# Kernel optimization log

Hardware: AMD Instinct MI355X
Metric: run time of the kernel (lower is better)

The kernel has to match this reference:

```python
import jax, jax.numpy as jnp
import numpy as np

WS = 8          # window size
DISP = 4        # ws // 2 cyclic shift displacement
WS2 = WS * WS   # tokens per window
HEADS = 3
HD = 32         # head dim
SCALE = HD ** -0.5


def _mask(upper_lower, left_right):
    m = np.zeros((WS2, WS2), np.float32)
    if upper_lower:
        m[-DISP * WS:, :-DISP * WS] = -np.inf
        m[:-DISP * WS, -DISP * WS:] = -np.inf
    if left_right:
        m = m.reshape(WS, WS, WS, WS)
        m[:, -DISP:, :, :-DISP] = -np.inf
        m[:, :-DISP, :, -DISP:] = -np.inf
        m = m.reshape(WS2, WS2)
    return m

UL = _mask(True, False)
LR = _mask(False, True)
_ix = np.array([(i, j) for i in range(WS) for j in range(WS)])
REL = (_ix[None] - _ix[:, None]) + WS - 1  # [WS2, WS2, 2] relative index table


def _ln(x, g, b):
    m = x.mean(-1, keepdims=True)
    v = ((x - m) ** 2).mean(-1, keepdims=True)
    return (x - m) * jax.lax.rsqrt(v + 1e-5) * g + b


def _wattn(x, Wqkv, pos, Wo, bo, shifted):
    if shifted:
        x = jnp.roll(x, (-DISP, -DISP), axis=(1, 2))
    b, H, W, _ = x.shape
    nh, nw = H // WS, W // WS
    # qkv: last dim laid out as (3, heads, head_dim) matching torch chunk + rearrange
    qkv = (x @ Wqkv).reshape(b, nh, WS, nw, WS, 3, HEADS, HD)
    qkv = qkv.transpose(5, 0, 6, 1, 3, 2, 4, 7).reshape(3, b, HEADS, nh * nw, WS2, HD)
    q, k, v = qkv[0], qkv[1], qkv[2]
    dots = jnp.einsum('bhwid,bhwjd->bhwij', q, k) * SCALE  # [b,h,nwin,ws2,ws2]
    dots = dots + pos[REL[..., 0], REL[..., 1]]            # relative pos bias
    if shifted:
        m = np.zeros((nh * nw, WS2, WS2), np.float32)
        m[-nw:] += UL             # windows in last row
        m[nw - 1::nw] += LR       # windows in last column
        dots = dots + jnp.asarray(m)[None, None]
    a = jax.nn.softmax(dots, axis=-1)
    o = jnp.einsum('bhwij,bhwjd->bhwid', a, v)
    o = o.reshape(b, HEADS, nh, nw, WS, WS, HD).transpose(0, 2, 4, 3, 5, 1, 6).reshape(b, H, W, HEADS * HD)
    o = o @ Wo + bo
    if shifted:
        o = jnp.roll(o, (DISP, DISP), axis=(1, 2))
    return o


def _block(t, g1, b1, Wqkv, pos, Wo, bo, g2, b2, W1, bf1, W2, bf2, shifted):
    t = t + _wattn(_ln(t, g1, b1), Wqkv, pos, Wo, bo, shifted)
    h = _ln(t, g2, b2)
    return t + (jax.nn.gelu(h @ W1 + bf1, approximate=False) @ W2 + bf2)


def _stage(x, Wm, bm, pa, pb):
    b, c, H, W = x.shape
    nh, nw = H // 2, W // 2
    # PatchMerging: Unfold(k=2,s=2) layout is (c, ki, kj) with c outermost
    t = x.reshape(b, c, nh, 2, nw, 2).transpose(0, 2, 4, 1, 3, 5).reshape(b, nh, nw, c * 4)
    t = t @ Wm + bm
    t = _block(t, *pa, False)
    t = _block(t, *pb, True)
    return t.transpose(0, 3, 1, 2)


def setup_inputs() -> dict:
    key = jax.random.key(0)
    ks = jax.random.split(key, 12)
    def w(k, shp):
        return jax.random.normal(k, shp, jnp.float32) * 0.02
    def blk(kw, kp, ko, k1, k2):
        return {'g1': jnp.ones((128,), jnp.float32), 'b1': jnp.zeros((128,), jnp.float32),
                'Wqkv': w(kw, (128, 288)), 'pos': jax.random.normal(kp, (15, 15), jnp.float32),
                'Wo': w(ko, (96, 128)), 'bo': jnp.zeros((128,), jnp.float32),
                'g2': jnp.ones((128,), jnp.float32), 'b2': jnp.zeros((128,), jnp.float32),
                'W1': w(k1, (128, 512)), 'bf1': jnp.zeros((512,), jnp.float32),
                'W2': w(k2, (512, 128)), 'bf2': jnp.zeros((128,), jnp.float32)}
    A = blk(ks[2], ks[3], ks[4], ks[5], ks[6])
    B = blk(ks[7], ks[8], ks[9], ks[10], ks[11])
    inp = {'x': jax.random.normal(ks[0], (8, 64, 256, 256), jnp.float32),
           'Wm': w(ks[1], (256, 128)), 'bm': jnp.zeros((128,), jnp.float32)}
    for n, v in A.items():
        inp[n + 'a'] = v
    for n, v in B.items():
        inp[n + 'b'] = v
    return inp


def reference(x, Wm, bm, g1a, b1a, Wqkva, posa, Woa, boa, g2a, b2a, W1a, bf1a, W2a, bf2a,
              g1b, b1b, Wqkvb, posb, Wob, bob, g2b, b2b, W1b, bf1b, W2b, bf2b):
    pa = (g1a, b1a, Wqkva, posa, Woa, boa, g2a, b2a, W1a, bf1a, W2a, bf2a)
    pb = (g1b, b1b, Wqkvb, posb, Wob, bob, g2b, b2b, W1b, bf1b, W2b, bf2b)
    return _stage(x, Wm, bm, pa, pb)
```

## Files before the change

kernel.cpp:

```cpp
#include <hip/hip_runtime.h>
#include <math.h>

#define Timg 131072
#define SCALE 0.17677669529663689f

typedef __attribute__((ext_vector_type(8))) short frag8;
typedef __attribute__((ext_vector_type(8))) unsigned short us8;
typedef __attribute__((ext_vector_type(4))) float f32x4;

__device__ inline float bf2f(unsigned short u) {
    union { unsigned int i; float f; } v; v.i = ((unsigned int)u) << 16; return v.f;
}
__device__ inline unsigned short f2bf(float f) {
    union { float f; unsigned int i; } v; v.f = f;
    unsigned int r = v.i + 0x7fff + ((v.i >> 16) & 1);
    return (unsigned short)(r >> 16);
}
__device__ inline unsigned int pk2(float lo, float hi) {
    return ((unsigned int)f2bf(hi) << 16) | (unsigned int)f2bf(lo);
}
__device__ inline float gelu_f(float x) {
    float u = x * x;
    float z = x * fmaf(u, 0.044715f, 1.0f);
    float e = __builtin_amdgcn_exp2f(-2.3025851f * z);
    return x * __builtin_amdgcn_rcpf(1.f + e);
}

__global__ __launch_bounds__(256) void k_wcvt(
    const float* __restrict__ src, unsigned short* __restrict__ dst, int R, int C,
    int qrows, float s)
{
    int idx = blockIdx.x * 256 + threadIdx.x;
    if (idx >= R * C) return;
    int r = idx / C, c = idx % C;
    float v = src[idx];
    if (c < qrows) v *= s;
    dst[(size_t)c * R + r] = f2bf(v);
}

#define LDA_PM 264
__global__ __launch_bounds__(256) void k_patchmerge(
    const float* __restrict__ x, const unsigned short* __restrict__ Wmt,
    const float* __restrict__ bm, float* __restrict__ t)
{
    __shared__ unsigned short A[64 * LDA_PM];
    int blk = blockIdx.x;
    int b   = blk >> 8;
    int rem = blk & 255;
    int h   = rem >> 1;
    int w0  = (rem & 1) * 64;
    int tid = threadIdx.x;
    {
        int row = tid >> 1, half = tid & 1;
        int c = row >> 1, ki = row & 1;
        const float* src = x + (((size_t)(b*64 + c))*256 + (size_t)(2*h + ki))*256 + 2*w0 + half*64;
        int base = c*4 + ki*2;
        #pragma unroll
        for (int q = 0; q < 16; ++q) {
            float4 v = *reinterpret_cast<const float4*>(src + q*4);
            int tk0 = (half*64 + q*4) >> 1;
            *reinterpret_cast<unsigned int*>(&A[ tk0     * LDA_PM + base]) = pk2(v.x, v.y);
            *reinterpret_cast<unsigned int*>(&A[(tk0 + 1)* LDA_PM + base]) = pk2(v.z, v.w);
        }
    }
    __syncthreads();
    int lane = tid & 63, w = tid >> 6;
    int lr = lane & 15, lg = lane >> 4;
    size_t tok0 = (size_t)blk * 64;
    #pragma unroll
    for (int nt = 0; nt < 2; ++nt) {
        int n0 = (w*2 + nt) * 16;
        f32x4 acc[4] = {};
        #pragma unroll
        for (int ks = 0; ks < 8; ++ks) {
            frag8 bfr = *reinterpret_cast<const frag8*>(Wmt + (size_t)(n0 + lr)*256 + ks*32 + lg*8);
            #pragma unroll
            for (int m = 0; m < 4; ++m) {
                frag8 af = *reinterpret_cast<const frag8*>(&A[(m*16 + lr)*LDA_PM + ks*32 + lg*8]);
                acc[m] = __builtin_amdgcn_mfma_f32_16x16x32_bf16(af, bfr, acc[m], 0, 0, 0);
            }
        }
        #pragma unroll
        for (int m = 0; m < 4; ++m)
            #pragma unroll
            for (int r = 0; r < 4; ++r) {
                int rowl = m*16 + lg*4 + r;
                int col  = n0 + lr;
                t[(tok0 + rowl)*128 + col] = acc[m][r] + bm[col];
            }
    }
}

#define LDQK 200
#define LDVT 72
#define LDP  72
#define LDAO 104
#define LDA  136
#define LDH  136
#define OFF_VT  25600
#define OFF_HC1 17408
#define R1SZ    39424
#define OFF_AO  48640
#define SMEMSZ  61952
__global__ __launch_bounds__(256) void k_block(
    const float* __restrict__ pos, float* __restrict__ t,
    const float* __restrict__ g1, const float* __restrict__ b1,
    const unsigned short* __restrict__ Wqt,
    const unsigned short* __restrict__ Wot, const float* __restrict__ bo,
    const float* __restrict__ g2, const float* __restrict__ b2,
    const unsigned short* __restrict__ W1t, const float* __restrict__ bf1,
    const unsigned short* __restrict__ W2t, const float* __restrict__ bf2,
    int shifted)
{
    __shared__ __attribute__((aligned(16))) char smem[SMEMSZ];
    __shared__ float stats[64][4][2];
    __shared__ float ps[225];
    unsigned short* QK   = (unsigned short*)(smem);
    unsigned short* Vt   = (unsigned short*)(smem + OFF_VT);
    unsigned short* Hc0  = (unsigned short*)(smem);
    unsigned short* Hc1  = (unsigned short*)(smem + OFF_HC1);
    unsigned short* Abuf = (unsigned short*)(smem + R1SZ);
    unsigned short* P    = (unsigned short*)(smem + R1SZ);
    unsigned short* ao   = (unsigned short*)(smem + OFF_AO);

    int blk = blockIdx.x;
    int b   = blk >> 8;
    int win = blk & 255;
    int wy  = win >> 4, wx = win & 15;
    int tid = threadIdx.x, lane = tid & 63, w = tid >> 6;
    int lr  = lane & 15, lg = lane >> 4;
    int sh  = shifted ? 4 : 0;

    for (int idx = tid; idx < 225; idx += 256) ps[idx] = pos[idx];

    #pragma unroll
    for (int it = 0; it < 16; ++it) {
        int m  = w*16 + it;
        int ir = m >> 3, ic = m & 7;
        int hh = (wy*8 + ir + sh) & 127, ww = (wx*8 + ic + sh) & 127;
        const float* p = t + ((size_t)((b*128 + hh)*128 + ww))*128;
        float2 v = *reinterpret_cast<const float2*>(p + lane*2);
        float s = v.x + v.y;
        #pragma unroll
        for (int o = 32; o; o >>= 1) s += __shfl_xor(s, o);
        float mean = s * 0.0078125f;
        float d0 = v.x - mean, d1 = v.y - mean;
        float q = d0*d0 + d1*d1;
        #pragma unroll
        for (int o = 32; o; o >>= 1) q += __shfl_xor(q, o);
        float rs = rsqrtf(q * 0.0078125f + 1e-5f);
        *reinterpret_cast<unsigned int*>(&Abuf[m*LDA + lane*2]) =
            pk2(d0*rs*g1[lane*2] + b1[lane*2], d1*rs*g1[lane*2+1] + b1[lane*2+1]);
    }
    __syncthreads();

    for (int nt = w; nt < 18; nt += 4) {
        f32x4 acc[4] = {};
        #pragma unroll
        for (int ks = 0; ks < 4; ++ks) {
            frag8 bfr = *reinterpret_cast<const frag8*>(Wqt + (size_t)(nt*16 + lr)*128 + ks*32 + lg*8);
            #pragma unroll
            for (int m = 0; m < 4; ++m) {
                frag8 af = *reinterpret_cast<const frag8*>(&Abuf[(m*16 + lr)*LDA + ks*32 + lg*8]);
                acc[m] = __builtin_amdgcn_mfma_f32_16x16x32_bf16(af, bfr, acc[m], 0, 0, 0);
            }
        }
        if (nt < 12) {
            #pragma unroll
            for (int m = 0; m < 4; ++m)
                #pragma unroll
                for (int r = 0; r < 4; ++r)
                    QK[(m*16 + lg*4 + r)*LDQK + nt*16 + lr] = f2bf(acc[m][r]);
        } else {
            #pragma unroll
            for (int m = 0; m < 4; ++m)
                #pragma unroll
                for (int r = 0; r < 4; ++r)
                    Vt[((nt - 12)*16 + lr)*LDVT + (m*16 + lg*4 + r)] = f2bf(acc[m][r]);
        }
    }
    __syncthreads();

    bool mUL = (shifted != 0) && (wy == 15);
    bool mLR = (shifted != 0) && (wx == 15);
    #pragma unroll 1
    for (int h = 0; h < 3; ++h) {
        frag8 qf = *reinterpret_cast<const frag8*>(&QK[(w*16 + lr)*LDQK + h*32 + lg*8]);
        f32x4 s[4];
        #pragma unroll
        for (int jt = 0; jt < 4; ++jt) {
            frag8 kf = *reinterpret_cast<const frag8*>(&QK[(jt*16 + lr)*LDQK + 96 + h*32 + lg*8]);
            f32x4 z = {0.f, 0.f, 0.f, 0.f};
            s[jt] = __builtin_amdgcn_mfma_f32_16x16x32_bf16(qf, kf, z, 0, 0, 0);
        }
        #pragma unroll
        for (int r = 0; r < 4; ++r) {
            int i  = w*16 + lg*4 + r;
            int ir = i >> 3, ic = i & 7;
            int ro = (7 - ir)*15 + (7 - ic);
            float vals[4]; float mx = -1e30f;
            #pragma unroll
            for (int jt = 0; jt < 4; ++jt) {
                int j = jt*16 + lr, jr = j >> 3, jc = j & 7;
                float val = s[jt][r] + ps[ro + jr*15 + jc];
                if ((mUL && ((jr >= 4) != (ir >= 4))) || (mLR && ((jc >= 4) != (ic >= 4)))) val = -1e30f;
                vals[jt] = val; mx = fmaxf(mx, val);
            }
            #pragma unroll
            for (int o = 8; o; o >>= 1) mx = fmaxf(mx, __shfl_xor(mx, o));
            float sum = 0.f;
            #pragma unroll
            for (int jt = 0; jt < 4; ++jt) { vals[jt] = __expf(vals[jt] - mx); sum += vals[jt]; }
            #pragma unroll
            for (int o = 8; o; o >>= 1) sum += __shfl_xor(sum, o);
            float inv = __builtin_amdgcn_rcpf(sum);
            #pragma unroll
            for (int jt = 0; jt < 4; ++jt)
                P[i*LDP + jt*16 + lr] = f2bf(vals[jt] * inv);
        }
        #pragma unroll
        for (int nd = 0; nd < 2; ++nd) {
            f32x4 o4 = {0.f, 0.f, 0.f, 0.f};
            #pragma unroll
            for (int kt = 0; kt < 2; ++kt) {
                frag8 pf = *reinterpret_cast<const frag8*>(&P[(w*16 + lr)*LDP + kt*32 + lg*8]);
                frag8 vf = *reinterpret_cast<const frag8*>(&Vt[(h*32 + nd*16 + lr)*LDVT + kt*32 + lg*8]);
                o4 = __builtin_amdgcn_mfma_f32_16x16x32_bf16(pf, vf, o4, 0, 0, 0);
            }
            #pragma unroll
            for (int r = 0; r < 4; ++r)
                ao[(w*16 + lg*4 + r)*LDAO + h*32 + nd*16 + lr] = f2bf(o4[r]);
        }
    }
    __syncthreads();

    f32x4 pacc[2][4] = {};
    #pragma unroll
    for (int ks = 0; ks < 3; ++ks) {
        frag8 bw0 = *reinterpret_cast<const frag8*>(Wot + (size_t)(w*32      + lr)*96 + ks*32 + lg*8);
        frag8 bw1 = *reinterpret_cast<const frag8*>(Wot + (size_t)(w*32 + 16 + lr)*96 + ks*32 + lg*8);
        #pragma unroll
        for (int m = 0; m < 4; ++m) {
            frag8 af = *reinterpret_cast<const frag8*>(&ao[(m*16 + lr)*LDAO + ks*32 + lg*8]);
            pacc[0][m] = __builtin_amdgcn_mfma_f32_16x16x32_bf16(af, bw0, pacc[0][m], 0, 0, 0);
            pacc[1][m] = __builtin_amdgcn_mfma_f32_16x16x32_bf16(af, bw1, pacc[1][m], 0, 0, 0);
        }
    }
    float t1[2][4][4];
    int   toks[4][4];
    #pragma unroll
    for (int m = 0; m < 4; ++m)
        #pragma unroll
        for (int r = 0; r < 4; ++r) {
            int rowl = m*16 + lg*4 + r;
            int ir = rowl >> 3, ic = rowl & 7;
            int hh = (wy*8 + ir + sh) & 127, ww = (wx*8 + ic + sh) & 127;
            toks[m][r] = (b*128 + hh)*128 + ww;
            #pragma unroll
            for (int nt = 0; nt < 2; ++nt) {
                int col = w*32 + nt*16 + lr;
                t1[nt][m][r] = t[(size_t)toks[m][r]*128 + col] + pacc[nt][m][r] + bo[col];
            }
        }
    #pragma unroll
    for (int m = 0; m < 4; ++m)
        #pragma unroll
        for (int r = 0; r < 4; ++r) {
            float v0 = t1[0][m][r], v1 = t1[1][m][r];
            float s = v0 + v1, q = v0*v0 + v1*v1;
            #pragma unroll
            for (int o = 8; o; o >>= 1) { s += __shfl_xor(s, o); q += __shfl_xor(q, o); }
            if (lr == 0) {
                int rowl = m*16 + lg*4 + r;
                stats[rowl][w][0] = s;
                stats[rowl][w][1] = q;
            }
        }
    __syncthreads();
    #pragma unroll
    for (int m = 0; m < 4; ++m)
        #pragma unroll
        for (int r = 0; r < 4; ++r) {
            int rowl = m*16 + lg*4 + r;
            float s = 0.f, q = 0.f;
            #pragma unroll
            for (int ww2 = 0; ww2 < 4; ++ww2) { s += stats[rowl][ww2][0]; q += stats[rowl][ww2][1]; }
            float mean = s * 0.0078125f;
            float var  = fmaxf(q * 0.0078125f - mean*mean, 0.f);
            float rs   = rsqrtf(var + 1e-5f);
            #pragma unroll
            for (int nt = 0; nt < 2; ++nt) {
                int col = w*32 + nt*16 + lr;
                Abuf[rowl*LDA + col] = f2bf((t1[nt][m][r] - mean)*rs*g2[col] + b2[col]);
            }
        }
    __syncthreads();

    f32x4 acc2[2][4] = {};
    #pragma unroll 1
    for (int kc = 0; kc < 4; ++kc) {
        unsigned short* Hc = (kc & 1) ? Hc1 : Hc0;
        #pragma unroll
        for (int nt = 0; nt < 2; ++nt) {
            int n0 = kc*128 + w*32 + nt*16;
            f32x4 a1[4] = {};
            #pragma unroll
            for (int ks = 0; ks < 4; ++ks) {
                frag8 bfr = *reinterpret_cast<const frag8*>(W1t + (size_t)(n0 + lr)*128 + ks*32 + lg*8);
                #pragma unroll
                for (int m = 0; m < 4; ++m) {
                    frag8 af = *reinterpret_cast<const frag8*>(&Abuf[(m*16 + lr)*LDA + ks*32 + lg*8]);
                    a1[m] = __builtin_amdgcn_mfma_f32_16x16x32_bf16(af, bfr, a1[m], 0, 0, 0);
                }
            }
            #pragma unroll
            for (int m = 0; m < 4; ++m)
                #pragma unroll
                for (int r = 0; r < 4; ++r) {
                    int rowl = m*16 + lg*4 + r;
                    int col  = w*32 + nt*16 + lr;
                    float xv = a1[m][r] + bf1[kc*128 + col];
                    Hc[rowl*LDH + col] = f2bf(gelu_f(xv));
                }
        }
        __syncthreads();
        #pragma unroll
        for (int nt = 0; nt < 2; ++nt) {
            int n0 = w*32 + nt*16;
            #pragma unroll
            for (int ks = 0; ks < 4; ++ks) {
                frag8 bfr = *reinterpret_cast<const frag8*>(W2t + (size_t)(n0 + lr)*512 + kc*128 + ks*32 + lg*8);
                #pragma unroll
                for (int m = 0; m < 4; ++m) {
                    frag8 hf = *reinterpret_cast<const frag8*>(&Hc[(m*16 + lr)*LDH + ks*32 + lg*8]);
                    acc2[nt][m] = __builtin_amdgcn_mfma_f32_16x16x32_bf16(hf, bfr, acc2[nt][m], 0, 0, 0);
                }
            }
        }
    }
    #pragma unroll
    for (int nt = 0; nt < 2; ++nt)
        #pragma unroll
        for (int m = 0; m < 4; ++m)
            #pragma unroll
            for (int r = 0; r < 4; ++r) {
                int col = w*32 + nt*16 + lr;
                t[(size_t)toks[m][r]*128 + col] = t1[nt][m][r] + acc2[nt][m][r] + bf2[col];
            }
}

__global__ __launch_bounds__(256) void k_transpose(
    const float* __restrict__ t, float* __restrict__ out)
{
    __shared__ float tile[128][33];
    int blk = blockIdx.x;
    int ct = blk & 3;
    int h  = (blk >> 2) & 127;
    int b  = blk >> 9;
    const float* src = t + ((size_t)b*16384 + (size_t)h*128)*128 + ct*32;
    #pragma unroll
    for (int q = 0; q < 16; ++q) {
        int idx = threadIdx.x + q*256;
        int w = idx >> 5, c = idx & 31;
        tile[w][c] = src[(size_t)w*128 + c];
    }
    __syncthreads();
    float* dst = out + ((size_t)(b*128 + ct*32))*16384 + (size_t)h*128;
    #pragma unroll
    for (int q = 0; q < 16; ++q) {
        int idx = threadIdx.x + q*256;
        int c = idx >> 7, w = idx & 127;
        dst[(size_t)c*16384 + w] = tile[w][c];
    }
}

extern "C" void kernel_launch(void* const* d_in, const int* in_sizes, int n_in,
                              void* d_out, int out_size, void* d_ws, size_t ws_size,
                              hipStream_t stream)
{
    const float* x  = (const float*)d_in[0];
    const float* Wm = (const float*)d_in[1];
    const float* bm = (const float*)d_in[2];

    float* t           = (float*)d_ws;
    unsigned short* wb = (unsigned short*)(t + (size_t)Timg*128);

    unsigned short* Wmt = wb;
    unsigned short* Wqt[2], *Wot[2], *W1t[2], *W2t[2];
    unsigned short* p = wb + 32768;
    for (int i = 0; i < 2; ++i) {
        Wqt[i] = p; p += 36864;
        Wot[i] = p; p += 12288;
        W1t[i] = p; p += 65536;
        W2t[i] = p; p += 65536;
    }

    k_wcvt<<<(256*128 + 255)/256, 256, 0, stream>>>(Wm, Wmt, 256, 128, 0, 1.f);
    for (int i = 0; i < 2; ++i) {
        k_wcvt<<<(128*288 + 255)/256, 256, 0, stream>>>((const float*)d_in[ 5 + i*12], Wqt[i], 128, 288, 96, SCALE);
        k_wcvt<<<( 96*128 + 255)/256, 256, 0, stream>>>((const float*)d_in[ 7 + i*12], Wot[i],  96, 128, 0, 1.f);
        k_wcvt<<<(128*512 + 255)/256, 256, 0, stream>>>((const float*)d_in[11 + i*12], W1t[i], 128, 512, 0, 1.f);
        k_wcvt<<<(512*128 + 255)/256, 256, 0, stream>>>((const float*)d_in[13 + i*12], W2t[i], 512, 128, 0, 1.f);
    }

    k_patchmerge<<<Timg/64, 256, 0, stream>>>(x, Wmt, bm, t);

    for (int blk = 0; blk < 2; ++blk) {
        const float* g1  = (const float*)d_in[ 3 + blk*12];
        const float* b1  = (const float*)d_in[ 4 + blk*12];
        const float* pos = (const float*)d_in[ 6 + blk*12];
        const float* bo  = (const float*)d_in[ 8 + blk*12];
        const float* g2  = (const float*)d_in[ 9 + blk*12];
        const float* b2  = (const float*)d_in[10 + blk*12];
        const float* bf1 = (const float*)d_in[12 + blk*12];
        const float* bf2 = (const float*)d_in[14 + blk*12];

        k_block<<<2048, 256, 0, stream>>>(pos, t, g1, b1, Wqt[blk],
                                          Wot[blk], bo, g2, b2,
                                          W1t[blk], bf1, W2t[blk], bf2, blk);
    }

    k_transpose<<<8*128*4, 256, 0, stream>>>(t, (float*)d_out);
}
```

Baseline: 407.1 us.

## Hoist residual loads early, vectorize LN1, and cache A fragments in registers

The residual rows of t are now loaded into registers at kernel start, so their global latency overlaps the LN/QKV/attention phases instead of stalling before the out-projection. LN1 is rewritten to use float4 loads with 16 lanes per token, a single-pass mean and variance, and packed 128-bit LDS stores. The A-operand MFMA fragments for QKV, the out-projection and FC1 are preloaded once into registers rather than reread from LDS for every n-tile, and the FC2 loop is reordered so each H fragment is read once per k-step. These changes raise register pressure a lot, which can lower occupancy or cause spills, and the single-pass variance is slightly less numerically robust.

Result: slower. 555.1 us (+36.4%).

```diff
diff --git a/kernel.cpp b/kernel.cpp
--- a/kernel.cpp
+++ b/kernel.cpp
@@ -7,6 +7,7 @@
 typedef __attribute__((ext_vector_type(8))) short frag8;
 typedef __attribute__((ext_vector_type(8))) unsigned short us8;
 typedef __attribute__((ext_vector_type(4))) float f32x4;
+typedef __attribute__((ext_vector_type(4))) unsigned int u32x4;
 
 __device__ inline float bf2f(unsigned short u) {
     union { unsigned int i; float f; } v; v.i = ((unsigned int)u) << 16; return v.f;
@@ -129,54 +130,88 @@
     int wy  = win >> 4, wx = win & 15;
     int tid = threadIdx.x, lane = tid & 63, w = tid >> 6;
     int lr  = lane & 15, lg = lane >> 4;
+    int l16 = lane & 15, quad = lane >> 4;
     int sh  = shifted ? 4 : 0;
 
     for (int idx = tid; idx < 225; idx += 256) ps[idx] = pos[idx];
 
-    #pragma unroll
-    for (int it = 0; it < 16; ++it) {
-        int m  = w*16 + it;
+    int toks[4][4];
+    #pragma unroll
+    for (int m = 0; m < 4; ++m)
+        #pragma unroll
+        for (int r = 0; r < 4; ++r) {
+            int rowl = m*16 + lg*4 + r;
+            int ir = rowl >> 3, ic = rowl & 7;
+            int hh = (wy*8 + ir + sh) & 127, ww = (wx*8 + ic + sh) & 127;
+            toks[m][r] = (b*128 + hh)*128 + ww;
+        }
+    float t1raw[2][4][4];
+    #pragma unroll
+    for (int nt = 0; nt < 2; ++nt)
+        #pragma unroll
+        for (int m = 0; m < 4; ++m)
+            #pragma unroll
+            for (int r = 0; r < 4; ++r)
+                t1raw[nt][m][r] = t[(size_t)toks[m][r]*128 + w*32 + nt*16 + lr];
+
+    float4 gv0 = *reinterpret_cast<const float4*>(g1 + l16*8);
+    float4 gv1 = *reinterpret_cast<const float4*>(g1 + l16*8 + 4);
+    float4 bv0 = *reinterpret_cast<const float4*>(b1 + l16*8);
+    float4 bv1 = *reinterpret_cast<const float4*>(b1 + l16*8 + 4);
+    #pragma unroll
+    for (int it2 = 0; it2 < 4; ++it2) {
+        int m  = w*16 + it2*4 + quad;
         int ir = m >> 3, ic = m & 7;
         int hh = (wy*8 + ir + sh) & 127, ww = (wx*8 + ic + sh) & 127;
-        const float* p = t + ((size_t)((b*128 + hh)*128 + ww))*128;
-        float2 v = *reinterpret_cast<const float2*>(p + lane*2);
-        float s = v.x + v.y;
-        #pragma unroll
-        for (int o = 32; o; o >>= 1) s += __shfl_xor(s, o);
+        const float* p = t + ((size_t)((b*128 + hh)*128 + ww))*128 + l16*8;
+        float4 v0 = *reinterpret_cast<const float4*>(p);
+        float4 v1 = *reinterpret_cast<const float4*>(p + 4);
+        float s = v0.x+v0.y+v0.z+v0.w + v1.x+v1.y+v1.z+v1.w;
+        float q = v0.x*v0.x+v0.y*v0.y+v0.z*v0.z+v0.w*v0.w
+                + v1.x*v1.x+v1.y*v1.y+v1.z*v1.z+v1.w*v1.w;
+        #pragma unroll
+        for (int o = 8; o; o >>= 1) { s += __shfl_xor(s, o); q += __shfl_xor(q, o); }
         float mean = s * 0.0078125f;
-        float d0 = v.x - mean, d1 = v.y - mean;
-        float q = d0*d0 + d1*d1;
-        #pragma unroll
-        for (int o = 32; o; o >>= 1) q += __shfl_xor(q, o);
-        float rs = rsqrtf(q * 0.0078125f + 1e-5f);
-        *reinterpret_cast<unsigned int*>(&Abuf[m*LDA + lane*2]) =
-            pk2(d0*rs*g1[lane*2] + b1[lane*2], d1*rs*g1[lane*2+1] + b1[lane*2+1]);
-    }
-    __syncthreads();
-
-    for (int nt = w; nt < 18; nt += 4) {
-        f32x4 acc[4] = {};
-        #pragma unroll
-        for (int ks = 0; ks < 4; ++ks) {
-            frag8 bfr = *reinterpret_cast<const frag8*>(Wqt + (size_t)(nt*16 + lr)*128 + ks*32 + lg*8);
-            #pragma unroll
-            for (int m = 0; m < 4; ++m) {
-                frag8 af = *reinterpret_cast<const frag8*>(&Abuf[(m*16 + lr)*LDA + ks*32 + lg*8]);
-                acc[m] = __builtin_amdgcn_mfma_f32_16x16x32_bf16(af, bfr, acc[m], 0, 0, 0);
-            }
-        }
-        if (nt < 12) {
+        float var  = fmaxf(q * 0.0078125f - mean*mean, 0.f);
+        float rs   = rsqrtf(var + 1e-5f);
+        u32x4 pk;
+        pk.x = pk2((v0.x-mean)*rs*gv0.x + bv0.x, (v0.y-mean)*rs*gv0.y + bv0.y);
+        pk.y = pk2((v0.z-mean)*rs*gv0.z + bv0.z, (v0.w-mean)*rs*gv0.w + bv0.w);
+        pk.z = pk2((v1.x-mean)*rs*gv1.x + bv1.x, (v1.y-mean)*rs*gv1.y + bv1.y);
+        pk.w = pk2((v1.z-mean)*rs*gv1.z + bv1.z, (v1.w-mean)*rs*gv1.w + bv1.w);
+        *reinterpret_cast<u32x4*>(&Abuf[m*LDA + l16*8]) = pk;
+    }
+    __syncthreads();
+
+    {
+        frag8 afq[4][4];
+        #pragma unroll
+        for (int ks = 0; ks < 4; ++ks)
             #pragma unroll
             for (int m = 0; m < 4; ++m)
-                #pragma unroll
-                for (int r = 0; r < 4; ++r)
-                    QK[(m*16 + lg*4 + r)*LDQK + nt*16 + lr] = f2bf(acc[m][r]);
-        } else {
-            #pragma unroll
-            for (int m = 0; m < 4; ++m)
-                #pragma unroll
-                for (int r = 0; r < 4; ++r)
-                    Vt[((nt - 12)*16 + lr)*LDVT + (m*16 + lg*4 + r)] = f2bf(acc[m][r]);
+                afq[ks][m] = *reinterpret_cast<const frag8*>(&Abuf[(m*16 + lr)*LDA + ks*32 + lg*8]);
+        for (int nt = w; nt < 18; nt += 4) {
+            f32x4 acc[4] = {};
+            #pragma unroll
+            for (int ks = 0; ks < 4; ++ks) {
+                frag8 bfr = *reinterpret_cast<const frag8*>(Wqt + (size_t)(nt*16 + lr)*128 + ks*32 + lg*8);
+                #pragma unroll
+                for (int m = 0; m < 4; ++m)
+                    acc[m] = __builtin_amdgcn_mfma_f32_16x16x32_bf16(afq[ks][m], bfr, acc[m], 0, 0, 0);
+            }
+            if (nt < 12) {
+                #pragma unroll
+                for (int m = 0; m < 4; ++m)
+                    #pragma unroll
+                    for (int r = 0; r < 4; ++r)
+                        QK[(m*16 + lg*4 + r)*LDQK + nt*16 + lr] = f2bf(acc[m][r]);
+            } else {
+                #pragma unroll
+                for (int m = 0; m < 4; ++m)
+                    #pragma unroll
+                    for (int r = 0; r < 4; ++r)
+                        Vt[((nt - 12)*16 + lr)*LDVT + (m*16 + lg*4 + r)] = f2bf(acc[m][r]);
+            }
         }
     }
     __syncthreads();
@@ -234,34 +269,35 @@
     }
     __syncthreads();
 
-    f32x4 pacc[2][4] = {};
-    #pragma unroll
-    for (int ks = 0; ks < 3; ++ks) {
-        frag8 bw0 = *reinterpret_cast<const frag8*>(Wot + (size_t)(w*32      + lr)*96 + ks*32 + lg*8);
-        frag8 bw1 = *reinterpret_cast<const frag8*>(Wot + (size_t)(w*32 + 16 + lr)*96 + ks*32 + lg*8);
-        #pragma unroll
-        for (int m = 0; m < 4; ++m) {
-            frag8 af = *reinterpret_cast<const frag8*>(&ao[(m*16 + lr)*LDAO + ks*32 + lg*8]);
-            pacc[0][m] = __builtin_amdgcn_mfma_f32_16x16x32_bf16(af, bw0, pacc[0][m], 0, 0, 0);
-            pacc[1][m] = __builtin_amdgcn_mfma_f32_16x16x32_bf16(af, bw1, pacc[1][m], 0, 0, 0);
-        }
-    }
     float t1[2][4][4];
-    int   toks[4][4];
-    #pragma unroll
-    for (int m = 0; m < 4; ++m)
-        #pragma unroll
-        for (int r = 0; r < 4; ++r) {
-            int rowl = m*16 + lg*4 + r;
-            int ir = rowl >> 3, ic = rowl & 7;
-            int hh = (wy*8 + ir + sh) & 127, ww = (wx*8 + ic + sh) & 127;
-            toks[m][r] = (b*128 + hh)*128 + ww;
-            #pragma unroll
-            for (int nt = 0; nt < 2; ++nt) {
-                int col = w*32 + nt*16 + lr;
-                t1[nt][m][r] = t[(size_t)toks[m][r]*128 + col] + pacc[nt][m][r] + bo[col];
-            }
-        }
+    {
+        frag8 afo[3][4];
+        #pragma unroll
+        for (int ks = 0; ks < 3; ++ks)
+            #pragma unroll
+            for (int m = 0; m < 4; ++m)
+                afo[ks][m] = *reinterpret_cast<const frag8*>(&ao[(m*16 + lr)*LDAO + ks*32 + lg*8]);
+        f32x4 pacc[2][4] = {};
+        #pragma unroll
+        for (int ks = 0; ks < 3; ++ks) {
+            frag8 bw0 = *reinterpret_cast<const frag8*>(Wot + (size_t)(w*32      + lr)*96 + ks*32 + lg*8);
+            frag8 bw1 = *reinterpret_cast<const frag8*>(Wot + (size_t)(w*32 + 16 + lr)*96 + ks*32 + lg*8);
+            #pragma unroll
+            for (int m = 0; m < 4; ++m) {
+                pacc[0][m] = __builtin_amdgcn_mfma_f32_16x16x32_bf16(afo[ks][m], bw0, pacc[0][m], 0, 0, 0);
+                pacc[1][m] = __builtin_amdgcn_mfma_f32_16x16x32_bf16(afo[ks][m], bw1, pacc[1][m], 0, 0, 0);
+            }
+        }
+        #pragma unroll
+        for (int nt = 0; nt < 2; ++nt) {
+            float bov = bo[w*32 + nt*16 + lr];
+            #pragma unroll
+            for (int m = 0; m < 4; ++m)
+                #pragma unroll
+                for (int r = 0; r < 4; ++r)
+                    t1[nt][m][r] = t1raw[nt][m][r] + pacc[nt][m][r] + bov;
+        }
+    }
     #pragma unroll
     for (int m = 0; m < 4; ++m)
         #pragma unroll
@@ -297,6 +333,12 @@
     __syncthreads();
 
     f32x4 acc2[2][4] = {};
+    frag8 af2[4][4];
+    #pragma unroll
+    for (int ks = 0; ks < 4; ++ks)
+        #pragma unroll
+        for (int m = 0; m < 4; ++m)
+            af2[ks][m] = *reinterpret_cast<const frag8*>(&Abuf[(m*16 + lr)*LDA + ks*32 + lg*8]);
     #pragma unroll 1
     for (int kc = 0; kc < 4; ++kc) {
         unsigned short* Hc = (kc & 1) ? Hc1 : Hc0;
@@ -308,10 +350,8 @@
             for (int ks = 0; ks < 4; ++ks) {
                 frag8 bfr = *reinterpret_cast<const frag8*>(W1t + (size_t)(n0 + lr)*128 + ks*32 + lg*8);
                 #pragma unroll
-                for (int m = 0; m < 4; ++m) {
-                    frag8 af = *reinterpret_cast<const frag8*>(&Abuf[(m*16 + lr)*LDA + ks*32 + lg*8]);
-                    a1[m] = __builtin_amdgcn_mfma_f32_16x16x32_bf16(af, bfr, a1[m], 0, 0, 0);
-                }
+                for (int m = 0; m < 4; ++m)
+                    a1[m] = __builtin_amdgcn_mfma_f32_16x16x32_bf16(af2[ks][m], bfr, a1[m], 0, 0, 0);
             }
             #pragma unroll
             for (int m = 0; m < 4; ++m)
@@ -325,28 +365,29 @@
         }
         __syncthreads();
         #pragma unroll
-        for (int nt = 0; nt < 2; ++nt) {
-            int n0 = w*32 + nt*16;
-            #pragma unroll
-            for (int ks = 0; ks < 4; ++ks) {
-                frag8 bfr = *reinterpret_cast<const frag8*>(W2t + (size_t)(n0 + lr)*512 + kc*128 + ks*32 + lg*8);
-                #pragma unroll
-                for (int m = 0; m < 4; ++m) {
-                    frag8 hf = *reinterpret_cast<const frag8*>(&Hc[(m*16 + lr)*LDH + ks*32 + lg*8]);
-                    acc2[nt][m] = __builtin_amdgcn_mfma_f32_16x16x32_bf16(hf, bfr, acc2[nt][m], 0, 0, 0);
-                }
-            }
-        }
-    }
-    #pragma unroll
-    for (int nt = 0; nt < 2; ++nt)
+        for (int ks = 0; ks < 4; ++ks) {
+            frag8 hfk[4];
+            #pragma unroll
+            for (int m = 0; m < 4; ++m)
+                hfk[m] = *reinterpret_cast<const frag8*>(&Hc[(m*16 + lr)*LDH + ks*32 + lg*8]);
+            #pragma unroll
+            for (int nt = 0; nt < 2; ++nt) {
+                frag8 bfr = *reinterpret_cast<const frag8*>(W2t + (size_t)(w*32 + nt*16 + lr)*512 + kc*128 + ks*32 + lg*8);
+                #pragma unroll
+                for (int m = 0; m < 4; ++m)
+                    acc2[nt][m] = __builtin_amdgcn_mfma_f32_16x16x32_bf16(hfk[m], bfr, acc2[nt][m], 0, 0, 0);
+            }
+        }
+    }
+    #pragma unroll
+    for (int nt = 0; nt < 2; ++nt) {
+        float bfv = bf2[w*32 + nt*16 + lr];
         #pragma unroll
         for (int m = 0; m < 4; ++m)
             #pragma unroll
-            for (int r = 0; r < 4; ++r) {
-                int col = w*32 + nt*16 + lr;
-                t[(size_t)toks[m][r]*128 + col] = t1[nt][m][r] + acc2[nt][m][r] + bf2[col];
-            }
+            for (int r = 0; r < 4; ++r)
+                t[(size_t)toks[m][r]*128 + w*32 + nt*16 + lr] = t1[nt][m][r] + acc2[nt][m][r] + bfv;
+    }
 }
 
 __global__ __launch_bounds__(256) void k_transpose(
```
